# Kernel tuning notes

Measured on AMD Instinct MI355X. Metric: run time of the kernel, lower is better.

Reference implementation:

```python
import jax, jax.numpy as jnp
import numpy as np

B, N, C, D, K, H, A = 4, 2048, 128, 128, 16, 64, 512


def _rn(k, shape, s):
    return (jax.random.normal(k, shape) * s).astype(jnp.float32)


def setup_inputs():
    ks = jax.random.split(jax.random.key(0), 40)
    w = lambda i, o, c: _rn(ks[i], (o, c), 0.02)
    b = lambda i, o: _rn(ks[i + 20], (o,), 0.02)
    p = {}
    p["xyz"] = _rn(ks[0], (B, 3, N), 1.0)
    p["pos"] = _rn(ks[1], (B, 2, N), 1.0)
    p["key"] = _rn(ks[2], (B, C, N), 1.0)
    p["query"] = _rn(ks[3], (B, C, N), 1.0)
    p["mv_w1"] = w(4, C, 2 * C); p["mv_b1"] = b(4, C)
    p["mv_w2"] = w(5, C, C);     p["mv_b2"] = b(5, C)
    p["mv_ws"] = w(6, C, 2 * C); p["mv_bs"] = b(6, C)
    p["wk"] = w(7, D, C); p["bk"] = b(7, D)
    p["wq"] = w(8, D, C); p["bq"] = b(8, D)
    p["wv"] = w(9, D, C); p["bv"] = b(9, D)
    p["xyz_w1"] = w(10, H, 3); p["xyz_b1"] = b(10, H)
    p["xyz_w2"] = w(11, D, H); p["xyz_b2"] = b(11, D)
    p["pos_w1"] = w(12, H, 2); p["pos_b1"] = b(12, H)
    p["pos_w2"] = w(13, D, H); p["pos_b2"] = b(13, D)
    p["xat_w1"] = w(14, A, D); p["xat_b1"] = b(14, A)
    p["xat_w2"] = w(15, D, A); p["xat_b2"] = b(15, D)
    p["at_w1"] = w(16, A, D); p["at_b1"] = b(16, A)
    p["at_w2"] = w(17, D, A); p["at_b2"] = b(17, D)
    p["wkq"] = w(18, C, D); p["bkq"] = b(18, C)
    p["wend"] = w(19, C, D); p["bend"] = b(19, C)
    return p


def c1(w, b, x):  # 1x1 Conv1d: (O,C) on (B,C,N)
    return jnp.einsum('oc,bcn->bon', w, x) + b[None, :, None]


def c2(w, b, x):  # 1x1 Conv2d: (O,C) on (B,C,N,K)
    return jnp.einsum('oc,bcnk->bonk', w, x) + b[None, :, None, None]


def mlp2(w1, b1, w2, b2, x):
    return c2(w2, b2, jax.nn.relu(c2(w1, b1, x)))


def softmax_one(x):  # exp(x-m) / (1 + sum exp(x-m)) over last axis
    m = jnp.max(x, axis=-1, keepdims=True)
    e = jnp.exp(x - m)
    return e / (1.0 + jnp.sum(e, axis=-1, keepdims=True))


def knn_idx(pts, k):  # pts: (B, N, d) -> (B, N, k) indices, include_self=True
    sq = jnp.sum(pts * pts, axis=-1)
    d2 = sq[:, :, None] + sq[:, None, :] - 2.0 * jnp.einsum('bnd,bmd->bnm', pts, pts)
    return jnp.argsort(d2, axis=-1)[:, :, :k]


def group(f, idx):  # f: (B,C,N), idx: (B,N,K) -> (B,C,N,K)
    return jax.vmap(lambda a, i: a[:, i])(f, idx)


def reference(xyz, pos, key, query, mv_w1, mv_b1, mv_w2, mv_b2, mv_ws, mv_bs,
              wk, bk, wq, bq, wv, bv, xyz_w1, xyz_b1, xyz_w2, xyz_b2,
              pos_w1, pos_b1, pos_w2, pos_b2, xat_w1, xat_b1, xat_w2, xat_b2,
              at_w1, at_b1, at_w2, at_b2, wkq, bkq, wend, bend):
    cat = jnp.concatenate([key, query], axis=1)  # (B, 2C, N)
    # MLP_Res
    value = c1(mv_w2, mv_b2, jax.nn.relu(c1(mv_w1, mv_b1, cat))) + c1(mv_ws, mv_bs, cat)
    identity = value
    k = c1(wk, bk, key)
    q = c1(wq, bq, query)
    v = c1(wv, bv, value)
    # ---- block 1: xyz-space kNN attention ----
    idx1 = knn_idx(jnp.swapaxes(xyz, 1, 2), K)           # (B,N,K)
    kq_rel = k[..., None] - group(q, idx1)               # (B,D,N,K)
    xyz_rel = xyz[..., None] - group(xyz, idx1)          # (B,3,N,K)
    xyz_emb = mlp2(xyz_w1, xyz_b1, xyz_w2, xyz_b2, xyz_rel)
    xa = softmax_one(mlp2(xat_w1, xat_b1, xat_w2, xat_b2, kq_rel + xyz_emb))
    agg = jnp.sum(xa * (v[..., None] + xyz_emb), axis=-1)  # (B,D,N)
    value = c1(wkq, bkq, agg) + identity
    value = c1(wv, bv, value)
    # ---- block 2: pos-space kNN attention ----
    idx2 = knn_idx(jnp.swapaxes(pos, 1, 2), K)
    qk_rel = q[..., None] - group(k, idx2)
    pos_rel = pos[..., None] - group(pos, idx2)
    pos_emb = mlp2(pos_w1, pos_b1, pos_w2, pos_b2, pos_rel)
    at = softmax_one(mlp2(at_w1, at_b1, at_w2, at_b2, qk_rel + pos_emb))
    agg = jnp.sum(at * (value[..., None] + pos_emb), axis=-1)
    y = c1(wend, bend, agg)
    return y + identity
```

## Files before the change

### kernel.cpp

```cpp
#include <hip/hip_runtime.h>
#include <hip/hip_bf16.h>

typedef __hip_bfloat16 bf16;
typedef unsigned long long ull;

#define BB 4
#define NN 2048
#define CCH 128
#define DDM 128
#define KNB 16
#define HHD 64
#define AAD 512
#define PP (BB*NN)

typedef __attribute__((ext_vector_type(8))) short short8;
typedef __attribute__((ext_vector_type(16))) float f32x16;

__device__ __forceinline__ float b2f(bf16 x) { return __bfloat162float(x); }
__device__ __forceinline__ bf16 f2b(float x) { return __float2bfloat16(x); }

__device__ __forceinline__ float ldany(const void* p, size_t i, int f32) {
  return f32 ? ((const float*)p)[i] : __bfloat162float(((const bf16*)p)[i]);
}

__device__ __forceinline__ long pack4(float a, float b, float c, float d) {
  union { bf16 h[4]; long l; } u;
  u.h[0] = f2b(a); u.h[1] = f2b(b); u.h[2] = f2b(c); u.h[3] = f2b(d);
  return u.l;
}
__device__ __forceinline__ void unpack4(long l, float* o) {
  union { bf16 h[4]; long l; } u; u.l = l;
  o[0] = b2f(u.h[0]); o[1] = b2f(u.h[1]); o[2] = b2f(u.h[2]); o[3] = b2f(u.h[3]);
}

__device__ __forceinline__ short8 ldfrag(const bf16* base, int row, int stride, int k0, int hl) {
  const bf16* p = base + (size_t)row * stride + k0 + (hl << 3);
  union { short8 v; long l[2]; } u;
  u.l[0] = *(const long*)p;
  u.l[1] = *(const long*)(p + 4);
  return u.v;
}

__device__ __forceinline__ f32x16 MFMA(short8 a, short8 b, f32x16 c) {
  return __builtin_amdgcn_mfma_f32_32x32x16_bf16(a, b, c, 0, 0, 0);
}

struct PtrArr { const void* p[36]; int n[36]; };
struct CvtTab { int src[16]; int off[16]; int n[16]; int isb[16]; };
struct G4 { const bf16* X[4]; int K[4]; int woff[4]; int boff[4]; bf16* out[4]; int relu[4]; };

__global__ __launch_bounds__(256) void sniff_kern(PtrArr pa, int* __restrict__ flags) {
  int t = blockIdx.x;
  const bf16* x = (const bf16*)pa.p[t];
  int n = pa.n[t]; if (n > 4096) n = 4096;
  __shared__ int cnt;
  if (threadIdx.x == 0) cnt = 0;
  __syncthreads();
  int c = 0;
  for (int i = threadIdx.x; i < n; i += 256) {
    float v = fabsf(__bfloat162float(x[i]));
    if (v == 0.f || (v >= 1e-6f && v <= 1024.f)) c++;
  }
  atomicAdd(&cnt, c);
  __syncthreads();
  if (threadIdx.x == 0) flags[t] = (cnt >= (n * 7) / 8) ? 0 : 1;
}

__global__ __launch_bounds__(256) void cvtprep_kern(PtrArr pa, CvtTab tab,
                                                    const int* __restrict__ flags,
                                                    bf16* __restrict__ warena, float* __restrict__ barena,
                                                    bf16* __restrict__ w1img0, bf16* __restrict__ w2img0,
                                                    bf16* __restrict__ cw2img0, float* __restrict__ fb0,
                                                    bf16* __restrict__ w1img1, bf16* __restrict__ w2img1,
                                                    bf16* __restrict__ cw2img1, float* __restrict__ fb1) {
  int y = blockIdx.y;
  if (y >= 2) {
    int e = y - 2;
    int i = blockIdx.x * 256 + threadIdx.x;
    if (i >= tab.n[e]) return;
    float v = ldany(pa.p[tab.src[e]], i, flags[tab.src[e]]);
    if (tab.isb[e]) barena[tab.off[e] + i] = v;
    else warena[tab.off[e] + i] = f2b(v);
    return;
  }
  int set = y;
  int cIdx = set ? 20 : 16, aIdx = set ? 28 : 24, dd = set ? 2 : 3;
  bf16* w1img = set ? w1img1 : w1img0;
  bf16* w2img = set ? w2img1 : w2img0;
  bf16* cw2img = set ? cw2img1 : cw2img0;
  float* fb = set ? fb1 : fb0;
  const void* cw1 = pa.p[cIdx];     const void* cb1 = pa.p[cIdx + 1];
  const void* cw2 = pa.p[cIdx + 2]; const void* cb2 = pa.p[cIdx + 3];
  const void* aw1 = pa.p[aIdx];     const void* ab1 = pa.p[aIdx + 1];
  const void* aw2 = pa.p[aIdx + 2]; const void* ab2 = pa.p[aIdx + 3];
  int i = blockIdx.x * 256 + threadIdx.x;
  const int fcw1 = flags[cIdx], fcb1 = flags[cIdx + 1];
  const int fcw2 = flags[cIdx + 2], fcb2 = flags[cIdx + 3];
  const int faw1 = flags[aIdx], fab1 = flags[aIdx + 1];
  const int faw2 = flags[aIdx + 2], fab2 = flags[aIdx + 3];
  float* ab1f = fb;
  float* ab2f = fb + 512;
  float* cb1f = fb + 640;
  float* cb2f = fb + 704;
  float* cw1f = fb + 832;
  if (i < 65536) {
    int hg = i >> 7, c = i & 127;
    w1img[(size_t)hg * 132 + c] = f2b(ldany(aw1, i, faw1));
  } else if (i < 131072) {
    int j = i - 65536;
    int o = j >> 9, hh = j & 511;
    int ac = hh >> 7, hloc = hh & 127;
    w2img[(size_t)(ac * 128 + o) * 132 + hloc] = f2b(ldany(aw2, j, faw2));
  } else if (i < 139264) {
    int j = i - 131072;
    int o = j >> 6, h = j & 63;
    cw2img[o * 68 + h] = f2b(ldany(cw2, j, fcw2));
  } else if (i < 139776) {
    int j = i - 139264; ab1f[j] = ldany(ab1, j, fab1);
  } else if (i < 139904) {
    int j = i - 139776; ab2f[j] = ldany(ab2, j, fab2);
  } else if (i < 139968) {
    int j = i - 139904; cb1f[j] = ldany(cb1, j, fcb1);
  } else if (i < 140096) {
    int j = i - 139968; cb2f[j] = ldany(cb2, j, fcb2);
  } else if (i < 140288) {
    int j = i - 140096;
    int h = j / 3, c = j % 3;
    cw1f[j] = (c < dd) ? ldany(cw1, h * dd + c, fcw1) : 0.f;
  }
}

__global__ __launch_bounds__(256) void trall_kern(const void* __restrict__ keyp,
                                                  const void* __restrict__ qryp,
                                                  const void* __restrict__ xyzp,
                                                  const void* __restrict__ posp,
                                                  const int* __restrict__ flags,
                                                  bf16* __restrict__ catT,
                                                  float* __restrict__ xyzT,
                                                  float* __restrict__ posT) {
  int bx = blockIdx.x;
  if (bx < 512) {
    __shared__ float tile[64][65];
    int xx = bx & 31, yy = (bx >> 5) & 1, zz = bx >> 6;
    int b = zz & 3, half = zz >> 2;
    const void* src = half ? qryp : keyp;
    const int f32 = flags[2 + half];
    int n0 = xx * 64, c0 = yy * 64;
    int tx = threadIdx.x & 63, ty = threadIdx.x >> 6;
    for (int r = ty; r < 64; r += 4)
      tile[r][tx] = ldany(src, (size_t)(b * 128 + c0 + r) * NN + n0 + tx, f32);
    __syncthreads();
    for (int r = ty; r < 64; r += 4)
      catT[(size_t)(b * NN + n0 + r) * 256 + half * 128 + c0 + tx] = __float2bfloat16(tile[tx][r]);
    return;
  }
  int cb = bx - 512;
  int which = cb >> 7;
  const void* src = which ? posp : xyzp;
  float* dst = which ? posT : xyzT;
  int dd = which ? 2 : 3;
  const int f32 = flags[which];
  int i = (cb & 127) * 256 * 2 + threadIdx.x;
  for (int rep = 0; rep < 2; ++rep, i += 256) {
    if (i < PP * 4) {
      int p = i >> 2, j = i & 3;
      int b = p >> 11, n = p & (NN - 1);
      dst[i] = (j < dd) ? ldany(src, (size_t)(b * dd + j) * NN + n, f32) : 0.f;
    }
  }
}

__global__ __launch_bounds__(256) void gemm4_kern(G4 g, const bf16* __restrict__ warena,
                                                  const float* __restrict__ barena) {
  __shared__ __attribute__((aligned(16))) bf16 XT[64 * 260];
  int op = blockIdx.y;
  const bf16* X = g.X[op];
  int K = g.K[op];
  const bf16* Wb = warena + g.woff[op];
  const float* bias = barena + g.boff[op];
  bf16* out = g.out[op];
  int relu = g.relu[op];
  int tid = threadIdx.x, lane = tid & 63, wv = tid >> 6;
  int hl = lane >> 5, cA = lane & 31;
  int p0 = blockIdx.x * 64;
  int SK = K + 4;
  int kc = K >> 3;
  for (int c = tid; c < 64 * kc; c += 256) {
    int r = c / kc, col = (c % kc) << 3;
    *(float4*)&XT[r * SK + col] = *(const float4*)&X[(size_t)(p0 + r) * 256 + col];
  }
  __syncthreads();
  int o0 = wv * 32;
  f32x16 acc[2];
#pragma unroll
  for (int r = 0; r < 16; ++r) {
    int o = o0 + (r & 3) + 8 * (r >> 2) + 4 * hl;
    float bv = bias[o];
    acc[0][r] = bv; acc[1][r] = bv;
  }
  for (int ks = 0; ks < (K >> 4); ++ks) {
    short8 af = ldfrag(Wb, o0 + cA, K, ks * 16, hl);
    short8 b0 = ldfrag(XT, cA, SK, ks * 16, hl);
    short8 b1 = ldfrag(XT, 32 + cA, SK, ks * 16, hl);
    acc[0] = MFMA(af, b0, acc[0]);
    acc[1] = MFMA(af, b1, acc[1]);
  }
#pragma unroll
  for (int t = 0; t < 2; ++t) {
    int m = p0 + t * 32 + cA;
#pragma unroll
    for (int q = 0; q < 4; ++q) {
      int ob = o0 + 8 * q + 4 * hl;
      float v[4] = {acc[t][4*q+0], acc[t][4*q+1], acc[t][4*q+2], acc[t][4*q+3]};
      if (relu) {
        v[0] = fmaxf(v[0], 0.f); v[1] = fmaxf(v[1], 0.f);
        v[2] = fmaxf(v[2], 0.f); v[3] = fmaxf(v[3], 0.f);
      }
      *(long*)(out + (size_t)m * 128 + ob) = pack4(v[0], v[1], v[2], v[3]);
    }
  }
}

__global__ __launch_bounds__(256) void gemm32_kern(
    const bf16* __restrict__ X,
    const bf16* __restrict__ Wb, const float* __restrict__ bias,
    const bf16* __restrict__ add, bf16* __restrict__ out, int relu,
    void* __restrict__ outT, const int* __restrict__ flags) {
  __shared__ __attribute__((aligned(16))) bf16 XT[32 * 132];
  int tid = threadIdx.x, lane = tid & 63, wv = tid >> 6;
  int hl = lane >> 5, cA = lane & 31;
  int p0 = blockIdx.x * 32;
  for (int c = tid; c < 32 * 16; c += 256) {
    int r = c >> 4, col = (c & 15) << 3;
    *(float4*)&XT[r * 132 + col] = *(const float4*)&X[(size_t)(p0 + r) * 128 + col];
  }
  __syncthreads();
  int o0 = wv * 32;
  f32x16 acc;
#pragma unroll
  for (int r = 0; r < 16; ++r) {
    int o = o0 + (r & 3) + 8 * (r >> 2) + 4 * hl;
    acc[r] = bias[o];
  }
#pragma unroll
  for (int ks = 0; ks < 8; ++ks) {
    short8 af = ldfrag(Wb, o0 + cA, 128, ks * 16, hl);
    short8 b0 = ldfrag(XT, cA, 132, ks * 16, hl);
    acc = MFMA(af, b0, acc);
  }
  int m = p0 + cA;
  int f32o = outT ? flags[2] : 0;
  int b = m >> 11, n = m & (NN - 1);
#pragma unroll
  for (int q = 0; q < 4; ++q) {
    int ob = o0 + 8 * q + 4 * hl;
    float v[4] = {acc[4*q+0], acc[4*q+1], acc[4*q+2], acc[4*q+3]};
    if (add) {
      float av[4];
      unpack4(*(const long*)(add + (size_t)m * 128 + ob), av);
      v[0] += av[0]; v[1] += av[1]; v[2] += av[2]; v[3] += av[3];
    }
    if (relu) {
      v[0] = fmaxf(v[0], 0.f); v[1] = fmaxf(v[1], 0.f);
      v[2] = fmaxf(v[2], 0.f); v[3] = fmaxf(v[3], 0.f);
    }
    if (outT) {
#pragma unroll
      for (int i = 0; i < 4; ++i) {
        size_t oi = (size_t)(b * 128 + ob + i) * NN + n;
        if (f32o) ((float*)outT)[oi] = v[i];
        else ((bf16*)outT)[oi] = f2b(v[i]);
      }
    } else {
      *(long*)(out + (size_t)m * 128 + ob) = pack4(v[0], v[1], v[2], v[3]);
    }
  }
}

__global__ __launch_bounds__(512) void knn_kern(const float* __restrict__ coordsT,
                                                int* __restrict__ idxout) {
  __shared__ __attribute__((aligned(16))) float4 cds[NN];
  int tid = threadIdx.x, lane = tid & 63, wv = tid >> 6;
  int p0 = blockIdx.x * 8, b = p0 >> 11;
  for (int j = tid; j < NN; j += 512)
    cds[j] = *(const float4*)&coordsT[((size_t)(b << 11) + j) * 4];
  __syncthreads();
  int p = p0 + wv, n = p & (NN - 1);
  float4 cc = cds[n];
  float sqi = __fadd_rn(__fadd_rn(__fmul_rn(cc.x, cc.x), __fmul_rn(cc.y, cc.y)),
                        __fmul_rn(cc.z, cc.z));
  ull t[16];
#pragma unroll
  for (int i = 0; i < 16; ++i) t[i] = ~0ull;
  for (int s = 0; s < 32; ++s) {
    int j = (s << 6) | lane;
    float4 q = cds[j];
    float sqj = __fadd_rn(__fadd_rn(__fmul_rn(q.x, q.x), __fmul_rn(q.y, q.y)),
                          __fmul_rn(q.z, q.z));
    float dt  = __fadd_rn(__fadd_rn(__fmul_rn(cc.x, q.x), __fmul_rn(cc.y, q.y)),
                          __fmul_rn(cc.z, q.z));
    float d2 = __fsub_rn(__fadd_rn(sqi, sqj), __fmul_rn(2.f, dt));
    unsigned u = __float_as_uint(d2);
    u = (u & 0x80000000u) ? ~u : (u | 0x80000000u);
    ull key = ((ull)u << 32) | (unsigned)j;
    if (key < t[15]) {
      t[15] = key;
#pragma unroll
      for (int i = 15; i > 0; --i) {
        ull lo = t[i - 1] < t[i] ? t[i - 1] : t[i];
        ull hi = t[i - 1] < t[i] ? t[i] : t[i - 1];
        t[i - 1] = lo; t[i] = hi;
      }
    }
  }
  for (int r = 0; r < KNB; ++r) {
    ull h = t[0];
    ull m = h;
#pragma unroll
    for (int off = 1; off < 64; off <<= 1) {
      ull o = __shfl_xor(m, off);
      m = o < m ? o : m;
    }
    if (lane == 0) idxout[(size_t)p * KNB + r] = (int)(m & 0xffffffffu);
    if (h == m) {
#pragma unroll
      for (int i = 0; i < 15; ++i) t[i] = t[i + 1];
      t[15] = ~0ull;
    }
  }
}

#define SMEM_BYTES 72192
__global__ __launch_bounds__(512, 4) void attn_mfma(
    const bf16* __restrict__ centerT, const bf16* __restrict__ gatherT,
    const float* __restrict__ coordsT, const bf16* __restrict__ vfeatT,
    const int* __restrict__ idx,
    const bf16* __restrict__ w1img, const bf16* __restrict__ w2img,
    const bf16* __restrict__ cw2img, const float* __restrict__ fb,
    bf16* __restrict__ aggT) {
  extern __shared__ char smem[];
  bf16* XS  = (bf16*)(smem);
  bf16* HT  = (bf16*)(smem + 33792);
  bf16* HC  = HT;
  bf16* CFE = (bf16*)(smem + 67584);
  bf16* VF  = (bf16*)(smem + 69632);
  int*  NID = (int*)(smem + 71680);
  const float* ab1f = fb;
  const float* ab2f = fb + 512;
  const float* cb1f = fb + 640;
  const float* cb2f = fb + 704;
  const float* cw1f = fb + 832;

  int tid = threadIdx.x, lane = tid & 63, wv = tid >> 6;
  int hl = lane >> 5, cA = lane & 31;
  int P0 = blockIdx.x * 8, b = P0 >> 11;

  if (tid < 128) NID[tid] = (b << 11) + idx[(size_t)(P0 + (tid >> 4)) * KNB + (tid & 15)];
  for (int i = tid; i < 1024; i += 512) {
    int g = i >> 7, d = i & 127;
    CFE[i] = centerT[(size_t)(P0 + g) * 128 + d];
    VF[i]  = vfeatT[(size_t)(P0 + g) * 128 + d];
  }
  __syncthreads();

  {
    int m = tid >> 2, sub = tid & 3;
    float4 ccd = *(const float4*)&coordsT[(size_t)(P0 + (m >> 4)) * 4];
    float4 nbd = *(const float4*)&coordsT[(size_t)NID[m] * 4];
    float r0 = ccd.x - nbd.x, r1 = ccd.y - nbd.y, r2 = ccd.z - nbd.z;
    int h0 = sub * 16;
    for (int hh = h0; hh < h0 + 16; hh += 4) {
      float a0 = fmaxf(cb1f[hh+0] + cw1f[(hh+0)*3]*r0 + cw1f[(hh+0)*3+1]*r1 + cw1f[(hh+0)*3+2]*r2, 0.f);
      float a1 = fmaxf(cb1f[hh+1] + cw1f[(hh+1)*3]*r0 + cw1f[(hh+1)*3+1]*r1 + cw1f[(hh+1)*3+2]*r2, 0.f);
      float a2 = fmaxf(cb1f[hh+2] + cw1f[(hh+2)*3]*r0 + cw1f[(hh+2)*3+1]*r1 + cw1f[(hh+2)*3+2]*r2, 0.f);
      float a3 = fmaxf(cb1f[hh+3] + cw1f[(hh+3)*3]*r0 + cw1f[(hh+3)*3+1]*r1 + cw1f[(hh+3)*3+2]*r2, 0.f);
      *(long*)&HC[m * 68 + hh] = pack4(a0, a1, a2, a3);
    }
    const bf16* grow = gatherT + (size_t)NID[m] * 128 + sub * 32;
    const bf16* crow = CFE + ((m >> 4) << 7) + sub * 32;
    for (int j = 0; j < 32; j += 4) {
      float gv[4], cv[4];
      unpack4(*(const long*)(grow + j), gv);
      unpack4(*(const long*)(crow + j), cv);
      *(long*)&XS[m * 132 + sub * 32 + j] =
          pack4(cv[0] - gv[0], cv[1] - gv[1], cv[2] - gv[2], cv[3] - gv[3]);
    }
  }
  __syncthreads();

  int r0s = (wv & 3) * 32;
  int mt0 = (wv >> 2) * 64;

  short8 pf[8];
#pragma unroll
  for (int ks = 0; ks < 8; ++ks)
    pf[ks] = ldfrag(w1img, r0s + cA, 132, ks * 16, hl);

  {
    f32x16 eacc[2];
#pragma unroll
    for (int r = 0; r < 16; ++r) {
      int o = r0s + (r & 3) + 8 * (r >> 2) + 4 * hl;
      float bv = cb2f[o];
      eacc[0][r] = bv; eacc[1][r] = bv;
    }
    for (int k0 = 0; k0 < 64; k0 += 16) {
      short8 af = ldfrag(cw2img, r0s + cA, 68, k0, hl);
      short8 b0 = ldfrag(HC, mt0 + cA, 68, k0, hl);
      short8 b1 = ldfrag(HC, mt0 + 32 + cA, 68, k0, hl);
      eacc[0] = MFMA(af, b0, eacc[0]);
      eacc[1] = MFMA(af, b1, eacc[1]);
    }
#pragma unroll
    for (int t = 0; t < 2; ++t) {
      int m = mt0 + t * 32 + cA;
#pragma unroll
      for (int q = 0; q < 4; ++q) {
        int ob = r0s + 8 * q + 4 * hl;
        bf16* px = &XS[m * 132 + ob];
        float xv[4];
        unpack4(*(long*)px, xv);
        *(long*)px = pack4(xv[0] + eacc[t][4*q+0], xv[1] + eacc[t][4*q+1],
                           xv[2] + eacc[t][4*q+2], xv[3] + eacc[t][4*q+3]);
      }
    }
  }
  __syncthreads();

  f32x16 acc2[2];
#pragma unroll
  for (int r = 0; r < 16; ++r) {
    int o = r0s + (r & 3) + 8 * (r >> 2) + 4 * hl;
    float bv = ab2f[o];
    acc2[0][r] = bv; acc2[1][r] = bv;
  }

  for (int ac = 0; ac < 4; ++ac) {
    const bf16* w2c = w2img + (size_t)ac * 16896;
    const bf16* w1n = w1img + (size_t)((ac + 1) & 3) * 16896;
    f32x16 acc1[2];
#pragma unroll
    for (int r = 0; r < 16; ++r) {
      int h = r0s + (r & 3) + 8 * (r >> 2) + 4 * hl;
      float bv = ab1f[ac * 128 + h];
      acc1[0][r] = bv; acc1[1][r] = bv;
    }
#pragma unroll
    for (int ks = 0; ks < 8; ++ks) {
      short8 af = pf[ks];
      short8 b0 = ldfrag(XS, mt0 + cA, 132, ks * 16, hl);
      short8 b1 = ldfrag(XS, mt0 + 32 + cA, 132, ks * 16, hl);
      pf[ks] = ldfrag(w2c, r0s + cA, 132, ks * 16, hl);
      acc1[0] = MFMA(af, b0, acc1[0]);
      acc1[1] = MFMA(af, b1, acc1[1]);
    }
    __syncthreads();
#pragma unroll
    for (int t = 0; t < 2; ++t) {
      int m = mt0 + t * 32 + cA;
#pragma unroll
      for (int q = 0; q < 4; ++q) {
        int hb = r0s + 8 * q + 4 * hl;
        *(long*)&HT[m * 132 + hb] =
            pack4(fmaxf(acc1[t][4*q+0], 0.f), fmaxf(acc1[t][4*q+1], 0.f),
                  fmaxf(acc1[t][4*q+2], 0.f), fmaxf(acc1[t][4*q+3], 0.f));
      }
    }
    __syncthreads();
#pragma unroll
    for (int ks = 0; ks < 8; ++ks) {
      short8 af = pf[ks];
      short8 b0 = ldfrag(HT, mt0 + cA, 132, ks * 16, hl);
      short8 b1 = ldfrag(HT, mt0 + 32 + cA, 132, ks * 16, hl);
      pf[ks] = ldfrag(w1n, r0s + cA, 132, ks * 16, hl);
      acc2[0] = MFMA(af, b0, acc2[0]);
      acc2[1] = MFMA(af, b1, acc2[1]);
    }
  }

  __syncthreads();
#pragma unroll
  for (int t = 0; t < 2; ++t) {
    int m = mt0 + t * 32 + cA;
#pragma unroll
    for (int q = 0; q < 4; ++q) {
      int ob = r0s + 8 * q + 4 * hl;
      *(long*)&HT[m * 132 + ob] = pack4(acc2[t][4*q+0], acc2[t][4*q+1],
                                        acc2[t][4*q+2], acc2[t][4*q+3]);
    }
  }
  __syncthreads();

  {
    int g = wv;
    int base = g * 16;
    float vbase0 = b2f(VF[g * 128 + lane])      - b2f(CFE[g * 128 + lane]);
    float vbase1 = b2f(VF[g * 128 + lane + 64]) - b2f(CFE[g * 128 + lane + 64]);
#pragma unroll
    for (int half = 0; half < 2; ++half) {
      int o = lane + half * 64;
      float vb = half ? vbase1 : vbase0;
      float e[16];
      float mx = -3.4e38f;
#pragma unroll
      for (int kk = 0; kk < 16; ++kk) {
        float x = b2f(HT[(base + kk) * 132 + o]);
        e[kk] = x;
        mx = fmaxf(mx, x);
      }
      float s = 0.f;
#pragma unroll
      for (int kk = 0; kk < 16; ++kk) { e[kk] = __expf(e[kk] - mx); s += e[kk]; }
      float inv = 1.f / (1.f + s);
      float acc = 0.f;
#pragma unroll
      for (int kk = 0; kk < 16; ++kk) {
        float xv = b2f(XS[(base + kk) * 132 + o]);
        float gv = b2f(gatherT[(size_t)NID[base + kk] * 128 + o]);
        acc += (e[kk] * inv) * (vb + xv + gv);
      }
      aggT[(size_t)(P0 + g) * 128 + o] = f2b(acc);
    }
  }
}

extern "C" void kernel_launch(void* const* d_in, const int* in_sizes, int n_in,
                              void* d_out, int out_size, void* d_ws, size_t ws_size,
                              hipStream_t stream) {
  int* flags = (int*)d_ws;
  bf16* catT = (bf16*)((float*)d_ws + 64);
  bf16* v0   = catT + (size_t)PP * 256;
  bf16* kT   = v0 + (size_t)PP * 128;
  bf16* qT   = kT + (size_t)PP * 128;
  bf16* sE   = qT + (size_t)PP * 128;
  bf16* sF   = sE + (size_t)PP * 128;
  bf16* sG   = sF + (size_t)PP * 128;
  float* xyzT = (float*)(sG + (size_t)PP * 128);
  float* posT = xyzT + (size_t)PP * 4;
  int* idxb = (int*)(posT + (size_t)PP * 4);
  bf16* w1i1 = (bf16*)(idxb + (size_t)PP * KNB);
  bf16* w2i1 = w1i1 + 67584;
  bf16* cw2i1 = w2i1 + 67584;
  bf16* w1i2 = cw2i1 + 8704;
  bf16* w2i2 = w1i2 + 67584;
  bf16* cw2i2 = w2i2 + 67584;
  float* fb1 = (float*)(cw2i2 + 8704);
  float* fb2 = fb1 + 1024;
  bf16* warena = (bf16*)(fb2 + 1024);
  float* barena = (float*)(warena + 163840);

  PtrArr pa;
  for (int i = 0; i < 36; ++i) { pa.p[i] = d_in[i]; pa.n[i] = in_sizes[i]; }
  sniff_kern<<<dim3(36), 256, 0, stream>>>(pa, flags);

  CvtTab tab;
  int wsrc[8] = {4, 8, 6, 10, 12, 14, 32, 34};
  int woff[8] = {0, 32768, 65536, 81920, 98304, 114688, 131072, 147456};
  int wn[8]   = {32768, 32768, 16384, 16384, 16384, 16384, 16384, 16384};
  int bsrc[8] = {5, 9, 7, 11, 13, 15, 33, 35};
  for (int e = 0; e < 8; ++e) {
    tab.src[e] = wsrc[e]; tab.off[e] = woff[e]; tab.n[e] = wn[e]; tab.isb[e] = 0;
    tab.src[8 + e] = bsrc[e]; tab.off[8 + e] = e * 128; tab.n[8 + e] = 128; tab.isb[8 + e] = 1;
  }
  cvtprep_kern<<<dim3(548, 18), 256, 0, stream>>>(pa, tab, flags, warena, barena,
                                                  w1i1, w2i1, cw2i1, fb1,
                                                  w1i2, w2i2, cw2i2, fb2);

  trall_kern<<<dim3(768), 256, 0, stream>>>(d_in[2], d_in[3], d_in[0], d_in[1],
                                            flags, catT, xyzT, posT);

  G4 g4;
  g4.X[0] = catT;       g4.K[0] = 256; g4.woff[0] = 0;      g4.boff[0] = 0;   g4.out[0] = sF; g4.relu[0] = 1;
  g4.X[1] = catT;       g4.K[1] = 256; g4.woff[1] = 32768;  g4.boff[1] = 128; g4.out[1] = sG; g4.relu[1] = 0;
  g4.X[2] = catT;       g4.K[2] = 128; g4.woff[2] = 81920;  g4.boff[2] = 384; g4.out[2] = kT; g4.relu[2] = 0;
  g4.X[3] = catT + 128; g4.K[3] = 128; g4.woff[3] = 98304;  g4.boff[3] = 512; g4.out[3] = qT; g4.relu[3] = 0;
  gemm4_kern<<<dim3(PP / 64, 4), 256, 0, stream>>>(g4, warena, barena);

  dim3 g32(PP / 32);
  gemm32_kern<<<g32, 256, 0, stream>>>(sF, warena + 65536,  barena + 256, sG,      v0, 0, nullptr, flags);
  gemm32_kern<<<g32, 256, 0, stream>>>(v0, warena + 114688, barena + 640, nullptr, sE, 0, nullptr, flags);

  hipFuncSetAttribute((const void*)attn_mfma, hipFuncAttributeMaxDynamicSharedMemorySize, SMEM_BYTES);

  knn_kern<<<dim3(PP / 8), 512, 0, stream>>>(xyzT, idxb);
  attn_mfma<<<dim3(PP / 8), 512, SMEM_BYTES, stream>>>(kT, qT, xyzT, sE, idxb,
                                                       w1i1, w2i1, cw2i1, fb1, sF);
  gemm32_kern<<<g32, 256, 0, stream>>>(sF, warena + 131072, barena + 768, v0,      sG, 0, nullptr, flags);
  gemm32_kern<<<g32, 256, 0, stream>>>(sG, warena + 114688, barena + 640, nullptr, sE, 0, nullptr, flags);
  knn_kern<<<dim3(PP / 8), 512, 0, stream>>>(posT, idxb);
  attn_mfma<<<dim3(PP / 8), 512, SMEM_BYTES, stream>>>(qT, kT, posT, sE, idxb,
                                                       w1i2, w2i2, cw2i2, fb2, sF);
  gemm32_kern<<<g32, 256, 0, stream>>>(sF, warena + 147456, barena + 896, v0, nullptr, 0, d_out, flags);
}
```

Before: 470.1 us.

## Merge both kNN launches into one grid and use bitonic sort per lane

```diff
diff --git a/kernel.cpp b/kernel.cpp
--- a/kernel.cpp
+++ b/kernel.cpp
@@ -277,9 +277,13 @@
   }
 }
 
-__global__ __launch_bounds__(512) void knn_kern(const float* __restrict__ coordsT,
-                                                int* __restrict__ idxout) {
+__global__ __launch_bounds__(512) void knn_kern(const float* __restrict__ xyzT,
+                                                const float* __restrict__ posT,
+                                                int* __restrict__ idx1,
+                                                int* __restrict__ idx2) {
   __shared__ __attribute__((aligned(16))) float4 cds[NN];
+  const float* coordsT = blockIdx.y ? posT : xyzT;
+  int* idxout = blockIdx.y ? idx2 : idx1;
   int tid = threadIdx.x, lane = tid & 63, wv = tid >> 6;
   int p0 = blockIdx.x * 8, b = p0 >> 11;
   for (int j = tid; j < NN; j += 512)
@@ -289,9 +293,8 @@
   float4 cc = cds[n];
   float sqi = __fadd_rn(__fadd_rn(__fmul_rn(cc.x, cc.x), __fmul_rn(cc.y, cc.y)),
                         __fmul_rn(cc.z, cc.z));
-  ull t[16];
-#pragma unroll
-  for (int i = 0; i < 16; ++i) t[i] = ~0ull;
+  ull t[32];
+#pragma unroll
   for (int s = 0; s < 32; ++s) {
     int j = (s << 6) | lane;
     float4 q = cds[j];
@@ -302,14 +305,23 @@
     float d2 = __fsub_rn(__fadd_rn(sqi, sqj), __fmul_rn(2.f, dt));
     unsigned u = __float_as_uint(d2);
     u = (u & 0x80000000u) ? ~u : (u | 0x80000000u);
-    ull key = ((ull)u << 32) | (unsigned)j;
-    if (key < t[15]) {
-      t[15] = key;
-#pragma unroll
-      for (int i = 15; i > 0; --i) {
-        ull lo = t[i - 1] < t[i] ? t[i - 1] : t[i];
-        ull hi = t[i - 1] < t[i] ? t[i] : t[i - 1];
-        t[i - 1] = lo; t[i] = hi;
+    t[s] = ((ull)u << 32) | (unsigned)j;
+  }
+#pragma unroll
+  for (int k = 2; k <= 32; k <<= 1) {
+#pragma unroll
+    for (int j = k >> 1; j > 0; j >>= 1) {
+#pragma unroll
+      for (int i = 0; i < 32; ++i) {
+        int l = i ^ j;
+        if (l > i) {
+          bool up = ((i & k) == 0);
+          ull a = t[i], c = t[l];
+          ull lo = a < c ? a : c;
+          ull hi = a < c ? c : a;
+          t[i] = up ? lo : hi;
+          t[l] = up ? hi : lo;
+        }
       }
     }
   }
@@ -537,8 +549,9 @@
   bf16* sG   = sF + (size_t)PP * 128;
   float* xyzT = (float*)(sG + (size_t)PP * 128);
   float* posT = xyzT + (size_t)PP * 4;
-  int* idxb = (int*)(posT + (size_t)PP * 4);
-  bf16* w1i1 = (bf16*)(idxb + (size_t)PP * KNB);
+  int* idx1 = (int*)(posT + (size_t)PP * 4);
+  int* idx2 = idx1 + (size_t)PP * KNB;
+  bf16* w1i1 = (bf16*)(idx2 + (size_t)PP * KNB);
   bf16* w2i1 = w1i1 + 67584;
   bf16* cw2i1 = w2i1 + 67584;
   bf16* w1i2 = cw2i1 + 8704;
@@ -569,6 +582,8 @@
   trall_kern<<<dim3(768), 256, 0, stream>>>(d_in[2], d_in[3], d_in[0], d_in[1],
                                             flags, catT, xyzT, posT);
 
+  knn_kern<<<dim3(PP / 8, 2), 512, 0, stream>>>(xyzT, posT, idx1, idx2);
+
   G4 g4;
   g4.X[0] = catT;       g4.K[0] = 256; g4.woff[0] = 0;      g4.boff[0] = 0;   g4.out[0] = sF; g4.relu[0] = 1;
   g4.X[1] = catT;       g4.K[1] = 256; g4.woff[1] = 32768;  g4.boff[1] = 128; g4.out[1] = sG; g4.relu[1] = 0;
@@ -582,13 +597,11 @@
 
   hipFuncSetAttribute((const void*)attn_mfma, hipFuncAttributeMaxDynamicSharedMemorySize, SMEM_BYTES);
 
-  knn_kern<<<dim3(PP / 8), 512, 0, stream>>>(xyzT, idxb);
-  attn_mfma<<<dim3(PP / 8), 512, SMEM_BYTES, stream>>>(kT, qT, xyzT, sE, idxb,
+  attn_mfma<<<dim3(PP / 8), 512, SMEM_BYTES, stream>>>(kT, qT, xyzT, sE, idx1,
                                                        w1i1, w2i1, cw2i1, fb1, sF);
   gemm32_kern<<<g32, 256, 0, stream>>>(sF, warena + 131072, barena + 768, v0,      sG, 0, nullptr, flags);
   gemm32_kern<<<g32, 256, 0, stream>>>(sG, warena + 114688, barena + 640, nullptr, sE, 0, nullptr, flags);
-  knn_kern<<<dim3(PP / 8), 512, 0, stream>>>(posT, idxb);
-  attn_mfma<<<dim3(PP / 8), 512, SMEM_BYTES, stream>>>(qT, kT, posT, sE, idxb,
+  attn_mfma<<<dim3(PP / 8), 512, SMEM_BYTES, stream>>>(qT, kT, posT, sE, idx2,
                                                        w1i2, w2i2, cw2i2, fb2, sF);
   gemm32_kern<<<g32, 256, 0, stream>>>(sF, warena + 147456, barena + 896, v0, nullptr, 0, d_out, flags);
 }
```

Result: faster. 392.9 us (-16.4%).
